# Kernel tuning notes

Hardware: AMD Instinct MI355X
Metric: run time of the kernel (lower is better)

Reference implementation:

```python
import jax, jax.numpy as jnp
import numpy as np

N = 50000      # nodes
E = 800000     # edges (before self loops)
DIN = 128      # input feature dim
H = 2          # attention heads
C = 64         # per-head hidden channels (hidden_dim)
HC = H * C     # 128, concat output width of each GATv2 layer
DOUT = 4       # NUM_LANES
NEG = 0.2      # GATv2 default negative_slope


def _w(key, fan_in, shape):
    return jax.random.normal(key, shape, dtype=jnp.float32) * (1.0 / np.sqrt(fan_in))


def setup_inputs() -> dict:
    key = jax.random.key(0)
    ks = jax.random.split(key, 32)
    inp = {
        "x": jax.random.normal(ks[0], (N, DIN), dtype=jnp.float32),
        "edge_index": jax.random.randint(ks[1], (2, E), 0, N, dtype=jnp.int64),
    }
    # layer 1: DIN -> H*C
    inp["W1l"] = _w(ks[2], DIN, (DIN, HC)); inp["b1l"] = jnp.zeros((HC,), jnp.float32)
    inp["W1r"] = _w(ks[3], DIN, (DIN, HC)); inp["b1r"] = jnp.zeros((HC,), jnp.float32)
    inp["att1"] = _w(ks[4], C, (H, C));     inp["bias1"] = jnp.zeros((HC,), jnp.float32)
    # layer 2: H*C -> H*C
    inp["W2l"] = _w(ks[5], HC, (HC, HC));   inp["b2l"] = jnp.zeros((HC,), jnp.float32)
    inp["W2r"] = _w(ks[6], HC, (HC, HC));   inp["b2r"] = jnp.zeros((HC,), jnp.float32)
    inp["att2"] = _w(ks[7], C, (H, C));     inp["bias2"] = jnp.zeros((HC,), jnp.float32)
    # layer 3: H*C -> H*C
    inp["W3l"] = _w(ks[8], HC, (HC, HC));   inp["b3l"] = jnp.zeros((HC,), jnp.float32)
    inp["W3r"] = _w(ks[9], HC, (HC, HC));   inp["b3r"] = jnp.zeros((HC,), jnp.float32)
    inp["att3"] = _w(ks[10], C, (H, C));    inp["bias3"] = jnp.zeros((HC,), jnp.float32)
    # output linear
    inp["Wout"] = _w(ks[11], HC, (HC, DOUT)); inp["bout"] = jnp.zeros((DOUT,), jnp.float32)
    return inp


def gat_layer(x, src, dst, Wl, bl, Wr, br, att, bias):
    # GATv2Conv, concat=True, add_self_loops already in src/dst.
    n = x.shape[0]
    h, c = att.shape
    xl = (x @ Wl + bl).reshape(n, h, c)   # source transform
    xr = (x @ Wr + br).reshape(n, h, c)   # target transform
    m = xl[src] + xr[dst]                               # [Etot, H, C]
    e = jnp.sum(jax.nn.leaky_relu(m, NEG) * att, -1)    # [Etot, H]
    emax = jax.ops.segment_max(e, dst, num_segments=n)  # segment softmax over in-edges
    p = jnp.exp(e - emax[dst])
    denom = jax.ops.segment_sum(p, dst, num_segments=n)
    alpha = p / denom[dst]                              # [Etot, H]
    out = jax.ops.segment_sum(alpha[:, :, None] * xl[src], dst, num_segments=n)
    return out.reshape(n, h * c) + bias


def reference(x, edge_index, W1l, b1l, W1r, b1r, att1, bias1,
              W2l, b2l, W2r, b2r, att2, bias2,
              W3l, b3l, W3r, b3r, att3, bias3, Wout, bout):
    n = x.shape[0]
    loop = jnp.arange(n, dtype=edge_index.dtype)
    src = jnp.concatenate([edge_index[0], loop])  # add self loops (PyG default)
    dst = jnp.concatenate([edge_index[1], loop])
    h = jax.nn.relu(gat_layer(x, src, dst, W1l, b1l, W1r, b1r, att1, bias1))
    h = jax.nn.relu(gat_layer(h, src, dst, W2l, b2l, W2r, b2r, att2, bias2))
    h = jax.nn.relu(gat_layer(h, src, dst, W3l, b3l, W3r, b3r, att3, bias3))
    return h @ Wout + bout
```

## Files before the change

kernel.cpp:

```cpp
#include <hip/hip_runtime.h>
#include <math.h>

#define DIN  128
#define HC   128
#define NEG  0.2f

typedef __attribute__((ext_vector_type(8))) short bf16x8;
typedef __attribute__((ext_vector_type(4))) float f32x4;
typedef __attribute__((ext_vector_type(4))) _Float16 half4;

__device__ __forceinline__ unsigned short f2bf_rne(float x) {
    unsigned u = __float_as_uint(x);
    unsigned r = u + 0x7FFFu + ((u >> 16) & 1u);
    return (unsigned short)(r >> 16);
}
__device__ __forceinline__ float bf2f(unsigned short h) {
    return __uint_as_float(((unsigned)h) << 16);
}

template <int CTRL>
__device__ __forceinline__ float dpp_xadd(float x) {
    int r = __builtin_amdgcn_update_dpp(0, __float_as_int(x), CTRL, 0xF, 0xF, true);
    return x + __int_as_float(r);
}
__device__ __forceinline__ float rowsum16(float x) {
    x = dpp_xadd<0xB1>(x);
    x = dpp_xadd<0x4E>(x);
    x = dpp_xadd<0x141>(x);
    x = dpp_xadd<0x140>(x);
    return x;
}

__global__ void hist_kernel(const int* __restrict__ ei, int E, int N,
                            int* __restrict__ counts) {
    int i = blockIdx.x * blockDim.x + threadIdx.x;
    int Etot = E + N;
    if (i >= Etot) return;
    int dst = (i < E) ? ei[E + i] : (i - E);
    if (dst < 0 || dst >= N) return;
    atomicAdd(&counts[dst], 1);
}

__global__ void scan_kernel(const int* __restrict__ counts,
                            int* __restrict__ rowptr,
                            int* __restrict__ cursor, int n) {
    __shared__ int wsum[16];
    int tid  = threadIdx.x;
    int lane = tid & 63, wid = tid >> 6;
    int running = 0;
    for (int base = 0; base < n; base += 4096) {
        int i = base + tid * 4;
        int4 v = make_int4(0, 0, 0, 0);
        if (i < n) v = *(const int4*)&counts[i];
        int ssum = v.x + v.y + v.z + v.w;
        int x = ssum;
        #pragma unroll
        for (int off = 1; off < 64; off <<= 1) {
            int y = __shfl_up(x, off, 64);
            if (lane >= off) x += y;
        }
        if (lane == 63) wsum[wid] = x;
        __syncthreads();
        if (tid < 16) {
            int w = wsum[tid];
            #pragma unroll
            for (int off = 1; off < 16; off <<= 1) {
                int y = __shfl_up(w, off, 64);
                if (tid >= off) w += y;
            }
            wsum[tid] = w;
        }
        __syncthreads();
        int excl = running + (wid ? wsum[wid - 1] : 0) + (x - ssum);
        if (i < n) {
            int4 r;
            r.x = excl;
            r.y = r.x + v.x;
            r.z = r.y + v.y;
            r.w = r.z + v.z;
            *(int4*)&rowptr[i] = r;
            *(int4*)&cursor[i] = r;
        }
        running += wsum[15];
        __syncthreads();
    }
    if (tid == 0) rowptr[n] = running;
}

__global__ void scatter_kernel(const int* __restrict__ ei, int E, int N,
                               int* __restrict__ cursor,
                               int* __restrict__ esrc) {
    int i = blockIdx.x * blockDim.x + threadIdx.x;
    int Etot = E + N;
    if (i >= Etot) return;
    int src = (i < E) ? ei[i]     : (i - E);
    int dst = (i < E) ? ei[E + i] : (i - E);
    if (dst < 0 || dst >= N || src < 0 || src >= N) return;
    int pos = atomicAdd(&cursor[dst], 1);
    esrc[pos] = src;
}

__global__ __launch_bounds__(256) void prep_w(
        const float* __restrict__ W1l, const float* __restrict__ W1r,
        const float* __restrict__ W2l, const float* __restrict__ W2r,
        const float* __restrict__ W3l, const float* __restrict__ W3r,
        unsigned short* __restrict__ hi, unsigned short* __restrict__ lo) {
    int m = blockIdx.y;
    const float* W = (m == 0) ? W1l : (m == 1) ? W1r : (m == 2) ? W2l
                   : (m == 3) ? W2r : (m == 4) ? W3l : W3r;
    int t = blockIdx.x * 256 + threadIdx.x;
    int kb = t >> 9, nf = (t >> 6) & 7, l = t & 63;
    int col = nf * 16 + (l & 15);
    int k0  = kb * 32 + (l >> 4) * 8;
    size_t ob = ((size_t)m * 2048 + t) * 8;
    #pragma unroll
    for (int j = 0; j < 8; ++j) {
        float v = W[(size_t)(k0 + j) * 128 + col];
        unsigned short h = f2bf_rne(v);
        hi[ob + j] = h;
        lo[ob + j] = f2bf_rne(v - bf2f(h));
    }
}

__global__ __launch_bounds__(256) void gemm_mfma_dual(
        const float* __restrict__ X,
        const unsigned short* __restrict__ Whi,
        const unsigned short* __restrict__ Wlo, int matbase,
        const float* __restrict__ bl, const float* __restrict__ br,
        _Float16* __restrict__ xlh, float* __restrict__ xr, int nrows) {
    const unsigned short* hpl = Whi + ((size_t)(matbase + 0) * 16384);
    const unsigned short* lpl = Wlo + ((size_t)(matbase + 0) * 16384);
    const unsigned short* hpr = Whi + ((size_t)(matbase + 1) * 16384);
    const unsigned short* lpr = Wlo + ((size_t)(matbase + 1) * 16384);

    int w   = threadIdx.x >> 6;
    int l   = threadIdx.x & 63;
    int m15 = l & 15, g = l >> 4;
    int rowbase = blockIdx.x * 64 + w * 16;

    f32x4 accl[8], accr[8];
    #pragma unroll
    for (int nf = 0; nf < 8; ++nf) {
        accl[nf] = (f32x4){0.f, 0.f, 0.f, 0.f};
        accr[nf] = (f32x4){0.f, 0.f, 0.f, 0.f};
    }

    #pragma unroll
    for (int kb = 0; kb < 4; ++kb) {
        int arow = rowbase + m15;
        float4 x0 = make_float4(0.f, 0.f, 0.f, 0.f), x1 = x0;
        if (arow < nrows) {
            const float* xp = &X[(size_t)arow * 128 + kb * 32 + g * 8];
            x0 = *(const float4*)xp;
            x1 = *(const float4*)(xp + 4);
        }
        float xv[8] = {x0.x, x0.y, x0.z, x0.w, x1.x, x1.y, x1.z, x1.w};
        bf16x8 ahi, alo;
        #pragma unroll
        for (int j = 0; j < 8; ++j) {
            unsigned short h = f2bf_rne(xv[j]);
            ahi[j] = (short)h;
            alo[j] = (short)f2bf_rne(xv[j] - bf2f(h));
        }
        #pragma unroll
        for (int nf = 0; nf < 8; ++nf) {
            size_t off = (((size_t)kb * 8 + nf) * 64 + l) * 8;
            bf16x8 bhl = *(const bf16x8*)&hpl[off];
            bf16x8 bll = *(const bf16x8*)&lpl[off];
            bf16x8 bhr = *(const bf16x8*)&hpr[off];
            bf16x8 blr = *(const bf16x8*)&lpr[off];
            accl[nf] = __builtin_amdgcn_mfma_f32_16x16x32_bf16(ahi, bhl, accl[nf], 0, 0, 0);
            accl[nf] = __builtin_amdgcn_mfma_f32_16x16x32_bf16(ahi, bll, accl[nf], 0, 0, 0);
            accl[nf] = __builtin_amdgcn_mfma_f32_16x16x32_bf16(alo, bhl, accl[nf], 0, 0, 0);
            accr[nf] = __builtin_amdgcn_mfma_f32_16x16x32_bf16(ahi, bhr, accr[nf], 0, 0, 0);
            accr[nf] = __builtin_amdgcn_mfma_f32_16x16x32_bf16(ahi, blr, accr[nf], 0, 0, 0);
            accr[nf] = __builtin_amdgcn_mfma_f32_16x16x32_bf16(alo, bhr, accr[nf], 0, 0, 0);
        }
    }

    #pragma unroll
    for (int nf = 0; nf < 8; ++nf) {
        int col = nf * 16 + m15;
        float vbl = bl[col];
        float vbr = br[col];
        #pragma unroll
        for (int r = 0; r < 4; ++r) {
            int row = rowbase + g * 4 + r;
            if (row < nrows) {
                xlh[(size_t)row * 128 + col] = (_Float16)(accl[nf][r] + vbl);
                xr[(size_t)row * 128 + col]  = accr[nf][r] + vbr;
            }
        }
    }
}

__device__ __forceinline__ float dsel(float4 a, float4 x, float4 tp, float4 tn) {
    float r, v;
    v = a.x + x.x; r  = v * (v > 0.f ? tp.x : tn.x);
    v = a.y + x.y; r += v * (v > 0.f ? tp.y : tn.y);
    v = a.z + x.z; r += v * (v > 0.f ? tp.z : tn.z);
    v = a.w + x.w; r += v * (v > 0.f ? tp.w : tn.w);
    return r;
}
__device__ __forceinline__ float4 h2f4(half4 h) {
    return make_float4((float)h.x, (float)h.y, (float)h.z, (float)h.w);
}

__global__ __launch_bounds__(256) void gat_aggregate(
        const _Float16* __restrict__ xlh, const float* __restrict__ xr,
        const int* __restrict__ rowptr, const int* __restrict__ esrc,
        const float* __restrict__ att, const float* __restrict__ bias,
        float* __restrict__ hout, int n, int do_relu,
        const float* __restrict__ Wout, const float* __restrict__ bout,
        float* __restrict__ out4) {
    int node = (int)((blockIdx.x * blockDim.x + threadIdx.x) >> 6);
    int lane = threadIdx.x & 63;
    if (node >= n) return;
    int g  = lane >> 4;
    int gl = lane & 15;
    int c0 = gl * 4;

    const float* xrp = &xr[(size_t)node * 128];
    float4 xr0 = *(const float4*)&xrp[c0];
    float4 xr1 = *(const float4*)&xrp[64 + c0];
    float4 atp0 = *(const float4*)&att[c0];
    float4 atp1 = *(const float4*)&att[64 + c0];
    float4 atn0 = make_float4(NEG * atp0.x, NEG * atp0.y, NEG * atp0.z, NEG * atp0.w);
    float4 atn1 = make_float4(NEG * atp1.x, NEG * atp1.y, NEG * atp1.z, NEG * atp1.w);

    float s0 = 0.f, s1 = 0.f;
    float4 acc0 = make_float4(0.f, 0.f, 0.f, 0.f);
    float4 acc1 = make_float4(0.f, 0.f, 0.f, 0.f);

    int pbeg = rowptr[node], pend = rowptr[node + 1];
    int p = pbeg + g;
    bool valid = p < pend;
    half4 h0c = (half4)(_Float16)0.f, h1c = (half4)(_Float16)0.f;
    if (valid) {
        const _Float16* xp = &xlh[(size_t)esrc[p] * 128];
        h0c = *(const half4*)&xp[c0];
        h1c = *(const half4*)&xp[64 + c0];
    }
    while (valid) {
        int  pn = p + 4;
        bool vn = pn < pend;
        half4 h0n = (half4)(_Float16)0.f, h1n = (half4)(_Float16)0.f;
        if (vn) {
            const _Float16* xp = &xlh[(size_t)esrc[pn] * 128];
            h0n = *(const half4*)&xp[c0];
            h1n = *(const half4*)&xp[64 + c0];
        }

        float4 a0 = h2f4(h0c), a1 = h2f4(h1c);
        float t0 = rowsum16(dsel(a0, xr0, atp0, atn0));
        float t1 = rowsum16(dsel(a1, xr1, atp1, atn1));
        float p0 = __expf(fminf(t0, 80.f));
        float p1 = __expf(fminf(t1, 80.f));
        s0 += p0;  s1 += p1;
        acc0.x += p0 * a0.x;  acc0.y += p0 * a0.y;
        acc0.z += p0 * a0.z;  acc0.w += p0 * a0.w;
        acc1.x += p1 * a1.x;  acc1.y += p1 * a1.y;
        acc1.z += p1 * a1.z;  acc1.w += p1 * a1.w;

        h0c = h0n; h1c = h1n; p = pn; valid = vn;
    }

    #pragma unroll
    for (int off = 16; off <= 32; off <<= 1) {
        s0 += __shfl_xor(s0, off, 64);
        s1 += __shfl_xor(s1, off, 64);
        acc0.x += __shfl_xor(acc0.x, off, 64); acc0.y += __shfl_xor(acc0.y, off, 64);
        acc0.z += __shfl_xor(acc0.z, off, 64); acc0.w += __shfl_xor(acc0.w, off, 64);
        acc1.x += __shfl_xor(acc1.x, off, 64); acc1.y += __shfl_xor(acc1.y, off, 64);
        acc1.z += __shfl_xor(acc1.z, off, 64); acc1.w += __shfl_xor(acc1.w, off, 64);
    }

    float inv0 = 1.f / s0, inv1 = 1.f / s1;

    if (out4) {
        float o0[4], o1[4];
        float a0v[4] = {acc0.x, acc0.y, acc0.z, acc0.w};
        float a1v[4] = {acc1.x, acc1.y, acc1.z, acc1.w};
        #pragma unroll
        for (int i = 0; i < 4; ++i) {
            o0[i] = a0v[i] * inv0 + bias[c0 + i];
            o1[i] = a1v[i] * inv1 + bias[64 + c0 + i];
            if (do_relu) { o0[i] = fmaxf(o0[i], 0.f); o1[i] = fmaxf(o1[i], 0.f); }
        }
        float p0 = 0.f, p1 = 0.f, p2 = 0.f, p3 = 0.f;
        #pragma unroll
        for (int i = 0; i < 4; ++i) {
            float4 w = *(const float4*)&Wout[(c0 + i) * 4];
            p0 += o0[i] * w.x; p1 += o0[i] * w.y; p2 += o0[i] * w.z; p3 += o0[i] * w.w;
        }
        #pragma unroll
        for (int i = 0; i < 4; ++i) {
            float4 w = *(const float4*)&Wout[(64 + c0 + i) * 4];
            p0 += o1[i] * w.x; p1 += o1[i] * w.y; p2 += o1[i] * w.z; p3 += o1[i] * w.w;
        }
        p0 = rowsum16(p0); p1 = rowsum16(p1);
        p2 = rowsum16(p2); p3 = rowsum16(p3);
        if (lane == 0) {
            float4 o = make_float4(p0 + bout[0], p1 + bout[1],
                                   p2 + bout[2], p3 + bout[3]);
            *(float4*)&out4[(size_t)node * 4] = o;
        }
        return;
    }

    if (g == 0) {
        float4 vb = *(const float4*)&bias[c0];
        float4 o = make_float4(acc0.x * inv0 + vb.x, acc0.y * inv0 + vb.y,
                               acc0.z * inv0 + vb.z, acc0.w * inv0 + vb.w);
        if (do_relu) {
            o.x = fmaxf(o.x, 0.f); o.y = fmaxf(o.y, 0.f);
            o.z = fmaxf(o.z, 0.f); o.w = fmaxf(o.w, 0.f);
        }
        *(float4*)&hout[(size_t)node * 128 + c0] = o;
    } else if (g == 1) {
        float4 vb = *(const float4*)&bias[64 + c0];
        float4 o = make_float4(acc1.x * inv1 + vb.x, acc1.y * inv1 + vb.y,
                               acc1.z * inv1 + vb.z, acc1.w * inv1 + vb.w);
        if (do_relu) {
            o.x = fmaxf(o.x, 0.f); o.y = fmaxf(o.y, 0.f);
            o.z = fmaxf(o.z, 0.f); o.w = fmaxf(o.w, 0.f);
        }
        *(float4*)&hout[(size_t)node * 128 + 64 + c0] = o;
    }
}

extern "C" void kernel_launch(void* const* d_in, const int* in_sizes, int n_in,
                              void* d_out, int out_size, void* d_ws,
                              size_t ws_size, hipStream_t stream) {
    const float* x    = (const float*)d_in[0];
    const int*   ei   = (const int*)  d_in[1];
    const float* W1l  = (const float*)d_in[2];
    const float* b1l  = (const float*)d_in[3];
    const float* W1r  = (const float*)d_in[4];
    const float* b1r  = (const float*)d_in[5];
    const float* att1 = (const float*)d_in[6];
    const float* bias1= (const float*)d_in[7];
    const float* W2l  = (const float*)d_in[8];
    const float* b2l  = (const float*)d_in[9];
    const float* W2r  = (const float*)d_in[10];
    const float* b2r  = (const float*)d_in[11];
    const float* att2 = (const float*)d_in[12];
    const float* bias2= (const float*)d_in[13];
    const float* W3l  = (const float*)d_in[14];
    const float* b3l  = (const float*)d_in[15];
    const float* W3r  = (const float*)d_in[16];
    const float* b3r  = (const float*)d_in[17];
    const float* att3 = (const float*)d_in[18];
    const float* bias3= (const float*)d_in[19];
    const float* Wout = (const float*)d_in[20];
    const float* bout = (const float*)d_in[21];

    int N    = in_sizes[0] / DIN;
    int E    = in_sizes[1] / 2;
    int Etot = E + N;

    char* base = (char*)d_ws;
    float* h = (float*)base;              base += (size_t)N * HC * 4;
    _Float16* xlh = (_Float16*)base;      base += (size_t)N * HC * 2;
    float* xr = (float*)base;             base += (size_t)N * HC * 4;
    unsigned short* whi = (unsigned short*)base;  base += 6 * 16384 * 2;
    unsigned short* wlo = (unsigned short*)base;  base += 6 * 16384 * 2;
    int* esrc   = (int*)base;             base += (size_t)Etot * 4;
    int* rowptr = (int*)base;             base += (size_t)(((N + 1) + 3) & ~3) * 4;
    int* cursor = (int*)base;             base += (size_t)N * 4;
    int* counts = (int*)base;

    hipMemsetAsync(counts, 0, (size_t)N * sizeof(int), stream);
    hist_kernel<<<(Etot + 255) / 256, 256, 0, stream>>>(ei, E, N, counts);
    scan_kernel<<<1, 1024, 0, stream>>>(counts, rowptr, cursor, N);
    scatter_kernel<<<(Etot + 255) / 256, 256, 0, stream>>>(ei, E, N, cursor, esrc);
    prep_w<<<dim3(8, 6), 256, 0, stream>>>(W1l, W1r, W2l, W2r, W3l, W3r, whi, wlo);

    int gemm_grid = (N + 63) / 64;
    int agg_grid  = (N + 3) / 4;

    gemm_mfma_dual<<<gemm_grid, 256, 0, stream>>>(x, whi, wlo, 0, b1l, b1r, xlh, xr, N);
    gat_aggregate<<<agg_grid, 256, 0, stream>>>(xlh, xr, rowptr, esrc, att1, bias1,
                                                h, N, 1, nullptr, nullptr, nullptr);
    gemm_mfma_dual<<<gemm_grid, 256, 0, stream>>>(h, whi, wlo, 2, b2l, b2r, xlh, xr, N);
    gat_aggregate<<<agg_grid, 256, 0, stream>>>(xlh, xr, rowptr, esrc, att2, bias2,
                                                h, N, 1, nullptr, nullptr, nullptr);
    gemm_mfma_dual<<<gemm_grid, 256, 0, stream>>>(h, whi, wlo, 4, b3l, b3r, xlh, xr, N);
    gat_aggregate<<<agg_grid, 256, 0, stream>>>(xlh, xr, rowptr, esrc, att3, bias3,
                                                nullptr, N, 1, Wout, bout,
                                                (float*)d_out);
}
```

Baseline: 356.4 us.

## Interleave head columns for 16-byte gathers, store xr as fp16, deepen prefetch

The GEMM epilogue now writes xl and xr in a permuted column order, so each lane's four channels from both heads sit next to each other. The aggregation kernel can then fetch them with a single 16-byte half8 load per edge instead of two 8-byte loads. xr is also stored in fp16 instead of fp32, which halves its write and read traffic. The edge loop now prefetches two edges ahead instead of one, to hide gather latency. Storing xr in fp16 adds rounding error to the attention logits, and the scattered 2-byte epilogue stores may coalesce worse.

```diff
diff --git a/kernel.cpp b/kernel.cpp
--- a/kernel.cpp
+++ b/kernel.cpp
@@ -7,7 +7,7 @@
 
 typedef __attribute__((ext_vector_type(8))) short bf16x8;
 typedef __attribute__((ext_vector_type(4))) float f32x4;
-typedef __attribute__((ext_vector_type(4))) _Float16 half4;
+typedef __attribute__((ext_vector_type(8))) _Float16 half8;
 
 __device__ __forceinline__ unsigned short f2bf_rne(float x) {
     unsigned u = __float_as_uint(x);
@@ -127,7 +127,7 @@
         const unsigned short* __restrict__ Whi,
         const unsigned short* __restrict__ Wlo, int matbase,
         const float* __restrict__ bl, const float* __restrict__ br,
-        _Float16* __restrict__ xlh, float* __restrict__ xr, int nrows) {
+        _Float16* __restrict__ xlh, _Float16* __restrict__ xrh, int nrows) {
     const unsigned short* hpl = Whi + ((size_t)(matbase + 0) * 16384);
     const unsigned short* lpl = Wlo + ((size_t)(matbase + 0) * 16384);
     const unsigned short* hpr = Whi + ((size_t)(matbase + 1) * 16384);
@@ -181,14 +181,15 @@
     #pragma unroll
     for (int nf = 0; nf < 8; ++nf) {
         int col = nf * 16 + m15;
+        int newpos = ((nf & 3) * 4 + (m15 >> 2)) * 8 + (nf >> 2) * 4 + (m15 & 3);
         float vbl = bl[col];
         float vbr = br[col];
         #pragma unroll
         for (int r = 0; r < 4; ++r) {
             int row = rowbase + g * 4 + r;
             if (row < nrows) {
-                xlh[(size_t)row * 128 + col] = (_Float16)(accl[nf][r] + vbl);
-                xr[(size_t)row * 128 + col]  = accr[nf][r] + vbr;
+                xlh[(size_t)row * 128 + newpos] = (_Float16)(accl[nf][r] + vbl);
+                xrh[(size_t)row * 128 + newpos] = (_Float16)(accr[nf][r] + vbr);
             }
         }
     }
@@ -202,12 +203,9 @@
     v = a.w + x.w; r += v * (v > 0.f ? tp.w : tn.w);
     return r;
 }
-__device__ __forceinline__ float4 h2f4(half4 h) {
-    return make_float4((float)h.x, (float)h.y, (float)h.z, (float)h.w);
-}
 
 __global__ __launch_bounds__(256) void gat_aggregate(
-        const _Float16* __restrict__ xlh, const float* __restrict__ xr,
+        const _Float16* __restrict__ xlh, const _Float16* __restrict__ xrh,
         const int* __restrict__ rowptr, const int* __restrict__ esrc,
         const float* __restrict__ att, const float* __restrict__ bias,
         float* __restrict__ hout, int n, int do_relu,
@@ -220,9 +218,11 @@
     int gl = lane & 15;
     int c0 = gl * 4;
 
-    const float* xrp = &xr[(size_t)node * 128];
-    float4 xr0 = *(const float4*)&xrp[c0];
-    float4 xr1 = *(const float4*)&xrp[64 + c0];
+    half8 xrh8 = *(const half8*)&xrh[(size_t)node * 128 + gl * 8];
+    float4 xr0 = make_float4((float)xrh8[0], (float)xrh8[1],
+                             (float)xrh8[2], (float)xrh8[3]);
+    float4 xr1 = make_float4((float)xrh8[4], (float)xrh8[5],
+                             (float)xrh8[6], (float)xrh8[7]);
     float4 atp0 = *(const float4*)&att[c0];
     float4 atp1 = *(const float4*)&att[64 + c0];
     float4 atn0 = make_float4(NEG * atp0.x, NEG * atp0.y, NEG * atp0.z, NEG * atp0.w);
@@ -234,24 +234,21 @@
 
     int pbeg = rowptr[node], pend = rowptr[node + 1];
     int p = pbeg + g;
-    bool valid = p < pend;
-    half4 h0c = (half4)(_Float16)0.f, h1c = (half4)(_Float16)0.f;
-    if (valid) {
-        const _Float16* xp = &xlh[(size_t)esrc[p] * 128];
-        h0c = *(const half4*)&xp[c0];
-        h1c = *(const half4*)&xp[64 + c0];
-    }
-    while (valid) {
-        int  pn = p + 4;
-        bool vn = pn < pend;
-        half4 h0n = (half4)(_Float16)0.f, h1n = (half4)(_Float16)0.f;
-        if (vn) {
-            const _Float16* xp = &xlh[(size_t)esrc[pn] * 128];
-            h0n = *(const half4*)&xp[c0];
-            h1n = *(const half4*)&xp[64 + c0];
-        }
-
-        float4 a0 = h2f4(h0c), a1 = h2f4(h1c);
+    bool v0 = p < pend;
+    bool v1 = p + 4 < pend;
+    half8 r0 = (half8)(_Float16)0.f, r1 = r0;
+    if (v0) r0 = *(const half8*)&xlh[(size_t)esrc[p] * 128 + gl * 8];
+    if (v1) r1 = *(const half8*)&xlh[(size_t)esrc[p + 4] * 128 + gl * 8];
+
+    while (v0) {
+        bool v2 = p + 8 < pend;
+        half8 r2 = (half8)(_Float16)0.f;
+        if (v2) r2 = *(const half8*)&xlh[(size_t)esrc[p + 8] * 128 + gl * 8];
+
+        float4 a0 = make_float4((float)r0[0], (float)r0[1],
+                                (float)r0[2], (float)r0[3]);
+        float4 a1 = make_float4((float)r0[4], (float)r0[5],
+                                (float)r0[6], (float)r0[7]);
         float t0 = rowsum16(dsel(a0, xr0, atp0, atn0));
         float t1 = rowsum16(dsel(a1, xr1, atp1, atn1));
         float p0 = __expf(fminf(t0, 80.f));
@@ -262,7 +259,7 @@
         acc1.x += p1 * a1.x;  acc1.y += p1 * a1.y;
         acc1.z += p1 * a1.z;  acc1.w += p1 * a1.w;
 
-        h0c = h0n; h1c = h1n; p = pn; valid = vn;
+        r0 = r1; r1 = r2; v0 = v1; v1 = v2; p += 4;
     }
 
     #pragma unroll
@@ -362,7 +359,7 @@
     char* base = (char*)d_ws;
     float* h = (float*)base;              base += (size_t)N * HC * 4;
     _Float16* xlh = (_Float16*)base;      base += (size_t)N * HC * 2;
-    float* xr = (float*)base;             base += (size_t)N * HC * 4;
+    _Float16* xrh = (_Float16*)base;      base += (size_t)N * HC * 2;
     unsigned short* whi = (unsigned short*)base;  base += 6 * 16384 * 2;
     unsigned short* wlo = (unsigned short*)base;  base += 6 * 16384 * 2;
     int* esrc   = (int*)base;             base += (size_t)Etot * 4;
@@ -379,14 +376,14 @@
     int gemm_grid = (N + 63) / 64;
     int agg_grid  = (N + 3) / 4;
 
-    gemm_mfma_dual<<<gemm_grid, 256, 0, stream>>>(x, whi, wlo, 0, b1l, b1r, xlh, xr, N);
-    gat_aggregate<<<agg_grid, 256, 0, stream>>>(xlh, xr, rowptr, esrc, att1, bias1,
+    gemm_mfma_dual<<<gemm_grid, 256, 0, stream>>>(x, whi, wlo, 0, b1l, b1r, xlh, xrh, N);
+    gat_aggregate<<<agg_grid, 256, 0, stream>>>(xlh, xrh, rowptr, esrc, att1, bias1,
                                                 h, N, 1, nullptr, nullptr, nullptr);
-    gemm_mfma_dual<<<gemm_grid, 256, 0, stream>>>(h, whi, wlo, 2, b2l, b2r, xlh, xr, N);
-    gat_aggregate<<<agg_grid, 256, 0, stream>>>(xlh, xr, rowptr, esrc, att2, bias2,
+    gemm_mfma_dual<<<gemm_grid, 256, 0, stream>>>(h, whi, wlo, 2, b2l, b2r, xlh, xrh, N);
+    gat_aggregate<<<agg_grid, 256, 0, stream>>>(xlh, xrh, rowptr, esrc, att2, bias2,
                                                 h, N, 1, nullptr, nullptr, nullptr);
-    gemm_mfma_dual<<<gemm_grid, 256, 0, stream>>>(h, whi, wlo, 4, b3l, b3r, xlh, xr, N);
-    gat_aggregate<<<agg_grid, 256, 0, stream>>>(xlh, xr, rowptr, esrc, att3, bias3,
+    gemm_mfma_dual<<<gemm_grid, 256, 0, stream>>>(h, whi, wlo, 4, b3l, b3r, xlh, xrh, N);
+    gat_aggregate<<<agg_grid, 256, 0, stream>>>(xlh, xrh, rowptr, esrc, att3, bias3,
                                                 nullptr, N, 1, Wout, bout,
                                                 (float*)d_out);
 }
```

Result: slower. 392.3 us (+10.1%).
